# Kernel optimization log

Hardware: AMD Instinct MI355X
Metric: run time of the kernel (lower is better)

Reference implementation:

```python
import jax, jax.numpy as jnp
import numpy as np


def setup_inputs() -> dict:
    key = jax.random.key(0)
    k1, k2, k3 = jax.random.split(key, 3)
    n, num_dim, classes = 65536, 1024, 1000
    inputs = jax.random.normal(k1, (n, num_dim), dtype=jnp.float32)
    targets = jax.random.randint(k2, (n,), 0, classes, dtype=jnp.int64)
    class_weight = jax.random.normal(k3, (classes, num_dim), dtype=jnp.float32)
    return {"inputs": inputs, "targets": targets, "classes": classes, "class_weight": class_weight}


def reference(inputs, targets, classes, class_weight):
    # Per-class mean (segment mean) for classes present in the batch;
    # absent classes fall back to the corresponding class_weight row.
    sums = jax.ops.segment_sum(inputs, targets, num_segments=classes)  # [classes, dim]
    counts = jax.ops.segment_sum(jnp.ones((inputs.shape[0],), inputs.dtype), targets, num_segments=classes)  # [classes]
    present = counts > 0
    means = sums / jnp.maximum(counts, 1.0)[:, None]
    centers = jnp.where(present[:, None], means, class_weight)
    return centers
```

## Files before the change

kernel.cpp:

```cpp
#include <hip/hip_runtime.h>


typedef float floatx4 __attribute__((ext_vector_type(4)));

__global__ void zero_kernel(int* __restrict__ p, int n) {
    int i = blockIdx.x * blockDim.x + threadIdx.x;
    if (i < n) p[i] = 0;
}

__global__ void count_kernel(const int* __restrict__ targets, int* __restrict__ counts, int n) {
    int i = blockIdx.x * blockDim.x + threadIdx.x;
    if (i < n) atomicAdd(&counts[targets[i]], 1);
}

__global__ void scan_kernel(const int* __restrict__ counts, int* __restrict__ offsets, int c) {
    __shared__ int buf[2][1024];
    int tid = threadIdx.x;
    int v = (tid < c) ? counts[tid] : 0;
    buf[0][tid] = v;
    __syncthreads();
    int src = 0;
    for (int d = 1; d < 1024; d <<= 1) {
        int x = buf[src][tid];
        if (tid >= d) x += buf[src][tid - d];
        buf[src ^ 1][tid] = x;
        src ^= 1;
        __syncthreads();
    }
    if (tid < c) offsets[tid] = buf[src][tid] - v;
}

__global__ void scatter_kernel(const int* __restrict__ targets,
                               const int* __restrict__ offsets,
                               int* __restrict__ cursors,
                               int* __restrict__ binned, int n) {
    int i = blockIdx.x * blockDim.x + threadIdx.x;
    if (i < n) {
        int t = targets[i];
        int pos = atomicAdd(&cursors[t], 1);
        binned[offsets[t] + pos] = i;
    }
}

__global__ void gather_kernel(const floatx4* __restrict__ in4,
                              const floatx4* __restrict__ w4,
                              const int* __restrict__ counts,
                              const int* __restrict__ offsets,
                              const int* __restrict__ binned,
                              floatx4* __restrict__ out4, int d4) {
    int c = blockIdx.x;
    int tid = threadIdx.x;
    int cnt = counts[c];
    size_t obase = (size_t)c * d4 + tid;
    if (cnt == 0) {
        out4[obase] = w4[obase];
        return;
    }
    __shared__ int rows[2048];
    int off = offsets[c];
    floatx4 a0 = {0,0,0,0}, a1 = {0,0,0,0}, a2 = {0,0,0,0}, a3 = {0,0,0,0};
    for (int base = 0; base < cnt; base += 2048) {
        int m = min(cnt - base, 2048);
        __syncthreads();
        for (int j = tid; j < m; j += blockDim.x) rows[j] = binned[off + base + j];
        __syncthreads();
        int j = 0;
        for (; j + 3 < m; j += 4) {
            int r0 = rows[j], r1 = rows[j+1], r2 = rows[j+2], r3 = rows[j+3];
            a0 += in4[(size_t)r0 * d4 + tid];
            a1 += in4[(size_t)r1 * d4 + tid];
            a2 += in4[(size_t)r2 * d4 + tid];
            a3 += in4[(size_t)r3 * d4 + tid];
        }
        for (; j < m; ++j) a0 += in4[(size_t)rows[j] * d4 + tid];
    }
    floatx4 s = (a0 + a1) + (a2 + a3);
    float inv = 1.0f / (float)cnt;
    out4[obase] = s * inv;
}

extern "C" void kernel_launch(void* const* d_in, const int* in_sizes, int n_in,
                              void* d_out, int out_size, void* d_ws, size_t ws_size,
                              hipStream_t stream) {
    const float* inputs = (const float*)d_in[0];
    const int* targets  = (const int*)d_in[1];
    const float* weight = (const float*)d_in[3];

    const int N = in_sizes[1];
    const int D = in_sizes[0] / N;
    const int C = in_sizes[3] / D;
    const int D4 = D / 4;

    int* counts  = (int*)d_ws;
    int* cursors = counts + C;
    int* offsets = cursors + C;
    int* binned  = offsets + C;

    zero_kernel<<<(2 * C + 255) / 256, 256, 0, stream>>>(counts, 2 * C);

    count_kernel<<<(N + 255) / 256, 256, 0, stream>>>(targets, counts, N);

    scan_kernel<<<1, 1024, 0, stream>>>(counts, offsets, C);

    scatter_kernel<<<(N + 255) / 256, 256, 0, stream>>>(targets, offsets, cursors, binned, N);

    gather_kernel<<<C, D4, 0, stream>>>(
        (const floatx4*)inputs, (const floatx4*)weight,
        counts, offsets, binned, (floatx4*)d_out, D4);
}
```

Measured before the change: 412.6 us.

## Split per-class gather across two blocks with partial sums and finalize

```diff
diff --git a/kernel.cpp b/kernel.cpp
--- a/kernel.cpp
+++ b/kernel.cpp
@@ -43,40 +43,67 @@
 }
 
 __global__ void gather_kernel(const floatx4* __restrict__ in4,
-                              const floatx4* __restrict__ w4,
                               const int* __restrict__ counts,
                               const int* __restrict__ offsets,
                               const int* __restrict__ binned,
-                              floatx4* __restrict__ out4, int d4) {
+                              floatx4* __restrict__ part4, int d4) {
+    int b = blockIdx.x;
+    int c = b >> 1, half = b & 1;
+    int cnt = counts[c];
+    if (cnt == 0) return;
+    int mid = (cnt + 1) >> 1;
+    int begin = half ? mid : 0;
+    int end   = half ? cnt : mid;
+    int off = offsets[c] + begin;
+    int m = end - begin;
+    int tid = threadIdx.x;
+
+    __shared__ int rows[1024];
+    floatx4 a0 = {0,0,0,0}, a1 = {0,0,0,0}, a2 = {0,0,0,0}, a3 = {0,0,0,0};
+    floatx4 a4 = {0,0,0,0}, a5 = {0,0,0,0}, a6 = {0,0,0,0}, a7 = {0,0,0,0};
+
+    for (int base = 0; base < m; base += 1024) {
+        int mm = min(m - base, 1024);
+        __syncthreads();
+        for (int j = tid; j < mm; j += blockDim.x) rows[j] = binned[off + base + j];
+        __syncthreads();
+        int j = 0;
+        for (; j + 7 < mm; j += 8) {
+            int r0 = rows[j],   r1 = rows[j+1], r2 = rows[j+2], r3 = rows[j+3];
+            int r4 = rows[j+4], r5 = rows[j+5], r6 = rows[j+6], r7 = rows[j+7];
+            a0 += __builtin_nontemporal_load(&in4[(size_t)r0 * d4 + tid]);
+            a1 += __builtin_nontemporal_load(&in4[(size_t)r1 * d4 + tid]);
+            a2 += __builtin_nontemporal_load(&in4[(size_t)r2 * d4 + tid]);
+            a3 += __builtin_nontemporal_load(&in4[(size_t)r3 * d4 + tid]);
+            a4 += __builtin_nontemporal_load(&in4[(size_t)r4 * d4 + tid]);
+            a5 += __builtin_nontemporal_load(&in4[(size_t)r5 * d4 + tid]);
+            a6 += __builtin_nontemporal_load(&in4[(size_t)r6 * d4 + tid]);
+            a7 += __builtin_nontemporal_load(&in4[(size_t)r7 * d4 + tid]);
+        }
+        for (; j < mm; ++j)
+            a0 += __builtin_nontemporal_load(&in4[(size_t)rows[j] * d4 + tid]);
+    }
+    floatx4 s = ((a0 + a1) + (a2 + a3)) + ((a4 + a5) + (a6 + a7));
+    part4[(size_t)b * d4 + tid] = s;
+}
+
+__global__ void finalize_kernel(const floatx4* __restrict__ part4,
+                                const floatx4* __restrict__ w4,
+                                const int* __restrict__ counts,
+                                floatx4* __restrict__ out4, int d4) {
     int c = blockIdx.x;
     int tid = threadIdx.x;
     int cnt = counts[c];
-    size_t obase = (size_t)c * d4 + tid;
-    if (cnt == 0) {
-        out4[obase] = w4[obase];
-        return;
+    size_t o = (size_t)c * d4 + tid;
+    floatx4 r;
+    if (cnt > 0) {
+        floatx4 s = part4[(size_t)(c << 1) * d4 + tid]
+                  + part4[(size_t)((c << 1) | 1) * d4 + tid];
+        r = s * (1.0f / (float)cnt);
+    } else {
+        r = w4[o];
     }
-    __shared__ int rows[2048];
-    int off = offsets[c];
-    floatx4 a0 = {0,0,0,0}, a1 = {0,0,0,0}, a2 = {0,0,0,0}, a3 = {0,0,0,0};
-    for (int base = 0; base < cnt; base += 2048) {
-        int m = min(cnt - base, 2048);
-        __syncthreads();
-        for (int j = tid; j < m; j += blockDim.x) rows[j] = binned[off + base + j];
-        __syncthreads();
-        int j = 0;
-        for (; j + 3 < m; j += 4) {
-            int r0 = rows[j], r1 = rows[j+1], r2 = rows[j+2], r3 = rows[j+3];
-            a0 += in4[(size_t)r0 * d4 + tid];
-            a1 += in4[(size_t)r1 * d4 + tid];
-            a2 += in4[(size_t)r2 * d4 + tid];
-            a3 += in4[(size_t)r3 * d4 + tid];
-        }
-        for (; j < m; ++j) a0 += in4[(size_t)rows[j] * d4 + tid];
-    }
-    floatx4 s = (a0 + a1) + (a2 + a3);
-    float inv = 1.0f / (float)cnt;
-    out4[obase] = s * inv;
+    out4[o] = r;
 }
 
 extern "C" void kernel_launch(void* const* d_in, const int* in_sizes, int n_in,
@@ -95,6 +122,7 @@
     int* cursors = counts + C;
     int* offsets = cursors + C;
     int* binned  = offsets + C;
+    float* part  = (float*)(binned + N);
 
     zero_kernel<<<(2 * C + 255) / 256, 256, 0, stream>>>(counts, 2 * C);
 
@@ -104,7 +132,9 @@
 
     scatter_kernel<<<(N + 255) / 256, 256, 0, stream>>>(targets, offsets, cursors, binned, N);
 
-    gather_kernel<<<C, D4, 0, stream>>>(
-        (const floatx4*)inputs, (const floatx4*)weight,
-        counts, offsets, binned, (floatx4*)d_out, D4);
+    gather_kernel<<<2 * C, D4, 0, stream>>>(
+        (const floatx4*)inputs, counts, offsets, binned, (floatx4*)part, D4);
+
+    finalize_kernel<<<C, D4, 0, stream>>>(
+        (const floatx4*)part, (const floatx4*)weight, counts, (floatx4*)d_out, D4);
 }
```

Measured after the change: 391.5 us. 1.05x faster.
